# Kernel tuning notes

Measured on AMD Instinct MI355X. Metric: run time of the kernel, lower is better.

## Reference

```python
import jax, jax.numpy as jnp
import numpy as np

N_NODES = 50000
N_EDGES = 640000
IN_DIM = 128
HID_DIM = 128


def setup_inputs() -> dict:
    key = jax.random.key(0)
    k1, k2, k3 = jax.random.split(key, 3)
    x = jax.random.normal(k1, (N_NODES, IN_DIM), dtype=jnp.float32)
    edge_index = jax.random.randint(k2, (2, N_EDGES), 0, N_NODES, dtype=jnp.int64)
    # GCNConv linear weight (glorot-ish scale) and bias
    W = jax.random.normal(k3, (IN_DIM, HID_DIM), dtype=jnp.float32) * (1.0 / np.sqrt(IN_DIM))
    b = jnp.zeros((HID_DIM,), dtype=jnp.float32)
    return {"x": x, "edge_index": edge_index, "W": W, "b": b}


def reference(x, edge_index, W, b):
    # PyG GCNConv: add self-loops, symmetric normalization deg^{-1/2} A deg^{-1/2},
    # linear transform, scatter-add aggregation, bias; then ReLU (SimpleGCN).
    N = x.shape[0]
    loops = jnp.arange(N, dtype=edge_index.dtype)
    src = jnp.concatenate([edge_index[0], loops])  # [E+N]
    dst = jnp.concatenate([edge_index[1], loops])  # [E+N]

    # degree of destination nodes (including self-loops)
    ones = jnp.ones(src.shape[0], dtype=x.dtype)
    deg = jax.ops.segment_sum(ones, dst, num_segments=N)  # [N]
    dinv = jnp.where(deg > 0, jax.lax.rsqrt(deg), 0.0)
    norm = dinv[src] * dinv[dst]  # [E+N]

    h = x @ W  # [N, H] dense GEMM first (PyG transforms before propagate)
    msg = h[src] * norm[:, None]  # gather + scale, [E+N, H]
    agg = jax.ops.segment_sum(msg, dst, num_segments=N)  # scatter-add, [N, H]
    return jax.nn.relu(agg + b)
```

## Files before the change

kernel.cpp:

```cpp
#include <hip/hip_runtime.h>
#include <cstdint>

#define NN 50000
#define NE 640000
#define DIM 128
#define CAP 64
#define GEMM_TILES ((NN + 63) / 64)
#define FILL_BLOCKS (NE / 4 / 256)
#define GATHER_BLOCKS (NN * 16 / 256)

typedef __attribute__((ext_vector_type(8))) short bf16x8;
typedef __attribute__((ext_vector_type(8))) unsigned short u16x8;
typedef __attribute__((ext_vector_type(4))) float f32x4;

static __device__ __forceinline__ short f2bf(float f) {
    union { float f; uint32_t u; } v; v.f = f;
    uint32_t r = v.u + 0x7FFFu + ((v.u >> 16) & 1u);
    return (short)(r >> 16);
}
static __device__ __forceinline__ float bf2f(unsigned short u) {
    union { uint32_t u; float f; } v; v.u = ((uint32_t)u) << 16;
    return v.f;
}

__global__ __launch_bounds__(256) void k_gemm(const float* __restrict__ x,
                                              const float* __restrict__ W,
                                              unsigned short* __restrict__ h_bf,
                                              int4* __restrict__ cnt4) {
    __shared__ bf16x8 Bs[2048];
    const int tid = threadIdx.x;
    const int gid = blockIdx.x * 256 + tid;
    if (gid < NN / 4) cnt4[gid] = make_int4(0, 0, 0, 0);

    #pragma unroll
    for (int i = 0; i < 8; ++i) {
        const int t = tid + i * 256;
        const int n = t >> 8;
        const int kk = (t >> 6) & 3;
        const int l = t & 63;
        const int c = n * 16 + (l & 15);
        const int k0 = kk * 32 + (l >> 4) * 8;
        bf16x8 v;
        #pragma unroll
        for (int j = 0; j < 8; ++j) v[j] = f2bf(W[(k0 + j) * DIM + c]);
        Bs[t] = v;
    }

    const int wave = tid >> 6;
    const int lane = tid & 63;
    const int rbase = blockIdx.x * 64 + wave * 16;
    const int rA = rbase + (lane & 15);
    const int kg = lane >> 4;

    bf16x8 a[4];
    if (rA < NN) {
        const float* xr = x + (size_t)rA * DIM + kg * 8;
        #pragma unroll
        for (int kk = 0; kk < 4; ++kk) {
            const float4 f0 = *reinterpret_cast<const float4*>(xr + kk * 32);
            const float4 f1 = *reinterpret_cast<const float4*>(xr + kk * 32 + 4);
            a[kk][0] = f2bf(f0.x); a[kk][1] = f2bf(f0.y);
            a[kk][2] = f2bf(f0.z); a[kk][3] = f2bf(f0.w);
            a[kk][4] = f2bf(f1.x); a[kk][5] = f2bf(f1.y);
            a[kk][6] = f2bf(f1.z); a[kk][7] = f2bf(f1.w);
        }
    } else {
        #pragma unroll
        for (int kk = 0; kk < 4; ++kk) a[kk] = (bf16x8)0;
    }
    __syncthreads();

    const int rC0 = rbase + (lane >> 4) * 4;
    const int col = lane & 15;
    #pragma unroll
    for (int n = 0; n < 8; ++n) {
        f32x4 acc = {0.f, 0.f, 0.f, 0.f};
        #pragma unroll
        for (int kk = 0; kk < 4; ++kk) {
            const bf16x8 b = Bs[(n * 4 + kk) * 64 + lane];
            acc = __builtin_amdgcn_mfma_f32_16x16x32_bf16(a[kk], b, acc, 0, 0, 0);
        }
        #pragma unroll
        for (int i = 0; i < 4; ++i) {
            const int r = rC0 + i;
            if (r < NN)
                h_bf[(size_t)r * DIM + n * 16 + col] = (unsigned short)f2bf(acc[i]);
        }
    }
}

__global__ __launch_bounds__(256) void k_fill(const int4* __restrict__ src4,
                                              const int4* __restrict__ dst4,
                                              int* __restrict__ cnt,
                                              int* __restrict__ srt) {
    const int i = blockIdx.x * 256 + threadIdx.x;
    const int4 s = src4[i];
    const int4 d = dst4[i];
    srt[((size_t)d.x << 6) + atomicAdd(&cnt[d.x], 1)] = s.x;
    srt[((size_t)d.y << 6) + atomicAdd(&cnt[d.y], 1)] = s.y;
    srt[((size_t)d.z << 6) + atomicAdd(&cnt[d.z], 1)] = s.z;
    srt[((size_t)d.w << 6) + atomicAdd(&cnt[d.w], 1)] = s.w;
}

__global__ __launch_bounds__(256) void k_gather(const int* __restrict__ cnt,
                                                const int* __restrict__ srt,
                                                const unsigned short* __restrict__ h_bf,
                                                const float* __restrict__ bias,
                                                float* __restrict__ out) {
    const int t = blockIdx.x * 256 + threadIdx.x;
    const int n = t >> 4;
    if (n >= NN) return;
    const int lane = t & 15;
    const u16x8* __restrict__ h8 = reinterpret_cast<const u16x8*>(h_bf);

    const int deg = cnt[n];
    const float did = rsqrtf((float)deg + 1.0f);

    float acc[8];
    {
        const u16x8 hv = h8[(size_t)n * 16 + lane];
        #pragma unroll
        for (int j = 0; j < 8; ++j) acc[j] = bf2f(hv[j]) * did;
    }

    const int* __restrict__ bucket = srt + ((size_t)n << 6);
    int p = 0;
    for (; p + 3 < deg; p += 4) {
        const int s0 = bucket[p],     s1 = bucket[p + 1];
        const int s2 = bucket[p + 2], s3 = bucket[p + 3];
        const float n0 = rsqrtf((float)cnt[s0] + 1.0f);
        const float n1 = rsqrtf((float)cnt[s1] + 1.0f);
        const float n2 = rsqrtf((float)cnt[s2] + 1.0f);
        const float n3 = rsqrtf((float)cnt[s3] + 1.0f);
        const u16x8 v0 = h8[(size_t)s0 * 16 + lane];
        const u16x8 v1 = h8[(size_t)s1 * 16 + lane];
        const u16x8 v2 = h8[(size_t)s2 * 16 + lane];
        const u16x8 v3 = h8[(size_t)s3 * 16 + lane];
        #pragma unroll
        for (int j = 0; j < 8; ++j) acc[j] = fmaf(bf2f(v0[j]), n0, acc[j]);
        #pragma unroll
        for (int j = 0; j < 8; ++j) acc[j] = fmaf(bf2f(v1[j]), n1, acc[j]);
        #pragma unroll
        for (int j = 0; j < 8; ++j) acc[j] = fmaf(bf2f(v2[j]), n2, acc[j]);
        #pragma unroll
        for (int j = 0; j < 8; ++j) acc[j] = fmaf(bf2f(v3[j]), n3, acc[j]);
    }
    for (; p < deg; ++p) {
        const int s0 = bucket[p];
        const float n0 = rsqrtf((float)cnt[s0] + 1.0f);
        const u16x8 v0 = h8[(size_t)s0 * 16 + lane];
        #pragma unroll
        for (int j = 0; j < 8; ++j) acc[j] = fmaf(bf2f(v0[j]), n0, acc[j]);
    }

    const float4 bv0 = reinterpret_cast<const float4*>(bias)[lane * 2];
    const float4 bv1 = reinterpret_cast<const float4*>(bias)[lane * 2 + 1];
    float4 o0, o1;
    o0.x = fmaxf(fmaf(did, acc[0], bv0.x), 0.f);
    o0.y = fmaxf(fmaf(did, acc[1], bv0.y), 0.f);
    o0.z = fmaxf(fmaf(did, acc[2], bv0.z), 0.f);
    o0.w = fmaxf(fmaf(did, acc[3], bv0.w), 0.f);
    o1.x = fmaxf(fmaf(did, acc[4], bv1.x), 0.f);
    o1.y = fmaxf(fmaf(did, acc[5], bv1.y), 0.f);
    o1.z = fmaxf(fmaf(did, acc[6], bv1.z), 0.f);
    o1.w = fmaxf(fmaf(did, acc[7], bv1.w), 0.f);
    float4* orow = reinterpret_cast<float4*>(out + (size_t)n * DIM) + lane * 2;
    orow[0] = o0;
    orow[1] = o1;
}

extern "C" void kernel_launch(void* const* d_in, const int* in_sizes, int n_in,
                              void* d_out, int out_size, void* d_ws, size_t ws_size,
                              hipStream_t stream) {
    const float* x  = (const float*)d_in[0];
    const int*   ei = (const int*)d_in[1];
    const float* W  = (const float*)d_in[2];
    const float* b  = (const float*)d_in[3];
    float* out = (float*)d_out;

    const int* src = ei;
    const int* dst = ei + NE;

    unsigned short* h_bf = (unsigned short*)d_ws;
    int* cnt = (int*)(h_bf + (size_t)NN * DIM);
    int* srt = cnt + NN;

    k_gemm<<<GEMM_TILES, 256, 0, stream>>>(x, W, h_bf, (int4*)cnt);
    k_fill<<<FILL_BLOCKS, 256, 0, stream>>>((const int4*)src, (const int4*)dst,
                                            cnt, srt);
    k_gather<<<GATHER_BLOCKS, 256, 0, stream>>>(cnt, srt, h_bf, b, out);
}
```

Before: 80.61 us.

## Store edge buckets as 16-bit indices and use packed bf16 conversion

The per-destination source buckets now hold 16-bit node indices instead of 32-bit ones. This relies on the node count fitting in 16 bits and is meant to halve bucket-array traffic in both the fill and gather kernels. The GEMM's manual fp32-to-bf16 rounding is also replaced with the HIP packed two-wide conversion intrinsic, to cut conversion instructions when staging W and x. The scattered 2-byte stores may not save as much memory traffic as the smaller footprint suggests.

```diff
diff --git a/kernel.cpp b/kernel.cpp
--- a/kernel.cpp
+++ b/kernel.cpp
@@ -1,4 +1,5 @@
 #include <hip/hip_runtime.h>
+#include <hip/hip_bf16.h>
 #include <cstdint>
 
 #define NN 50000
@@ -13,6 +14,14 @@
 typedef __attribute__((ext_vector_type(8))) unsigned short u16x8;
 typedef __attribute__((ext_vector_type(4))) float f32x4;
 
+union bfpack { bf16x8 v; uint32_t u[4]; };
+
+static __device__ __forceinline__ uint32_t pk2bf(float lo, float hi) {
+    __hip_bfloat162 t = __float22bfloat162_rn(make_float2(lo, hi));
+    union { __hip_bfloat162 b; uint32_t u; } v;
+    v.b = t;
+    return v.u;
+}
 static __device__ __forceinline__ short f2bf(float f) {
     union { float f; uint32_t u; } v; v.f = f;
     uint32_t r = v.u + 0x7FFFu + ((v.u >> 16) & 1u);
@@ -40,10 +49,12 @@
         const int l = t & 63;
         const int c = n * 16 + (l & 15);
         const int k0 = kk * 32 + (l >> 4) * 8;
-        bf16x8 v;
-        #pragma unroll
-        for (int j = 0; j < 8; ++j) v[j] = f2bf(W[(k0 + j) * DIM + c]);
-        Bs[t] = v;
+        const float* wc = W + (size_t)k0 * DIM + c;
+        bfpack t8;
+        #pragma unroll
+        for (int j = 0; j < 4; ++j)
+            t8.u[j] = pk2bf(wc[(2 * j) * DIM], wc[(2 * j + 1) * DIM]);
+        Bs[t] = t8.v;
     }
 
     const int wave = tid >> 6;
@@ -59,10 +70,12 @@
         for (int kk = 0; kk < 4; ++kk) {
             const float4 f0 = *reinterpret_cast<const float4*>(xr + kk * 32);
             const float4 f1 = *reinterpret_cast<const float4*>(xr + kk * 32 + 4);
-            a[kk][0] = f2bf(f0.x); a[kk][1] = f2bf(f0.y);
-            a[kk][2] = f2bf(f0.z); a[kk][3] = f2bf(f0.w);
-            a[kk][4] = f2bf(f1.x); a[kk][5] = f2bf(f1.y);
-            a[kk][6] = f2bf(f1.z); a[kk][7] = f2bf(f1.w);
+            bfpack t8;
+            t8.u[0] = pk2bf(f0.x, f0.y);
+            t8.u[1] = pk2bf(f0.z, f0.w);
+            t8.u[2] = pk2bf(f1.x, f1.y);
+            t8.u[3] = pk2bf(f1.z, f1.w);
+            a[kk] = t8.v;
         }
     } else {
         #pragma unroll
@@ -92,18 +105,18 @@
 __global__ __launch_bounds__(256) void k_fill(const int4* __restrict__ src4,
                                               const int4* __restrict__ dst4,
                                               int* __restrict__ cnt,
-                                              int* __restrict__ srt) {
+                                              unsigned short* __restrict__ srt) {
     const int i = blockIdx.x * 256 + threadIdx.x;
     const int4 s = src4[i];
     const int4 d = dst4[i];
-    srt[((size_t)d.x << 6) + atomicAdd(&cnt[d.x], 1)] = s.x;
-    srt[((size_t)d.y << 6) + atomicAdd(&cnt[d.y], 1)] = s.y;
-    srt[((size_t)d.z << 6) + atomicAdd(&cnt[d.z], 1)] = s.z;
-    srt[((size_t)d.w << 6) + atomicAdd(&cnt[d.w], 1)] = s.w;
+    srt[((size_t)d.x << 6) + atomicAdd(&cnt[d.x], 1)] = (unsigned short)s.x;
+    srt[((size_t)d.y << 6) + atomicAdd(&cnt[d.y], 1)] = (unsigned short)s.y;
+    srt[((size_t)d.z << 6) + atomicAdd(&cnt[d.z], 1)] = (unsigned short)s.z;
+    srt[((size_t)d.w << 6) + atomicAdd(&cnt[d.w], 1)] = (unsigned short)s.w;
 }
 
 __global__ __launch_bounds__(256) void k_gather(const int* __restrict__ cnt,
-                                                const int* __restrict__ srt,
+                                                const unsigned short* __restrict__ srt,
                                                 const unsigned short* __restrict__ h_bf,
                                                 const float* __restrict__ bias,
                                                 float* __restrict__ out) {
@@ -123,7 +136,7 @@
         for (int j = 0; j < 8; ++j) acc[j] = bf2f(hv[j]) * did;
     }
 
-    const int* __restrict__ bucket = srt + ((size_t)n << 6);
+    const unsigned short* __restrict__ bucket = srt + ((size_t)n << 6);
     int p = 0;
     for (; p + 3 < deg; p += 4) {
         const int s0 = bucket[p],     s1 = bucket[p + 1];
@@ -183,7 +196,7 @@
 
     unsigned short* h_bf = (unsigned short*)d_ws;
     int* cnt = (int*)(h_bf + (size_t)NN * DIM);
-    int* srt = cnt + NN;
+    unsigned short* srt = (unsigned short*)(cnt + NN);
 
     k_gemm<<<GEMM_TILES, 256, 0, stream>>>(x, W, h_bf, (int4*)cnt);
     k_fill<<<FILL_BLOCKS, 256, 0, stream>>>((const int4*)src, (const int4*)dst,
```

After: 79.53 us. Within noise of the previous version (-1.3%).
